# Kernel tuning notes

Hardware: AMD Instinct MI355X
Metric: run time of the kernel (lower is better)

## Reference

```python
import math
import jax, jax.numpy as jnp
import numpy as np

NUM_LAYERS = 2
D = 128
H = 8
CTX = 16
B, M, T = 4, 16, 256


def _lin(x, W, b):
    # torch nn.Linear: y = x @ W^T + b, W: [out, in]
    return jnp.einsum('...d,ed->...e', x, W) + b


def _ln(x, g, b, eps=1e-6):
    mu = jnp.mean(x, axis=-1, keepdims=True)
    v = jnp.mean((x - mu) ** 2, axis=-1, keepdims=True)
    return (x - mu) / jnp.sqrt(v + eps) * g + b


def _context_attention(x, L):
    # Faithful vectorization of the per-position python loop in ContextAttention.
    # Zero left-padding is NOT masked in the softmax (pad keys give score 0),
    # exactly as in the torch original.
    b, m, t, d = x.shape
    xp = jnp.pad(x, ((0, 0), (0, 0), (L - 1, 0), (0, 0)))  # [b,m,t+L-1,d]
    idx = jnp.arange(t)[:, None] + jnp.arange(L)[None, :]   # [t,L] window indices
    win = xp[:, :, idx, :]                                  # [b,m,t,L,d]
    scores = jnp.einsum('bmtd,bmtld->bmtl', x, win) / math.sqrt(d)
    w = jax.nn.softmax(scores, axis=-1)
    return jnp.einsum('bmtl,bmtld->bmtd', w, win)


def setup_inputs():
    key = jax.random.key(0)
    ks = jax.random.split(key, 8)
    L = NUM_LAYERS

    def w(k, shape):
        return jax.random.normal(k, shape, dtype=jnp.float32) * 0.02

    return {
        'x': jax.random.normal(ks[0], (B, M, T, D), dtype=jnp.float32),
        'Wq': w(ks[1], (L, D, D)), 'bq': jnp.zeros((L, D), jnp.float32),
        'Wk': w(ks[2], (L, D, D)), 'bk': jnp.zeros((L, D), jnp.float32),
        'Wv': w(ks[3], (L, D, D)), 'bv': jnp.zeros((L, D), jnp.float32),
        'Wo': w(ks[4], (L, D, D)), 'bo': jnp.zeros((L, D), jnp.float32),
        'W1': w(ks[5], (L, 4 * D, D)), 'b1': jnp.zeros((L, 4 * D), jnp.float32),
        'W2': w(ks[6], (L, D, 4 * D)), 'b2': jnp.zeros((L, D), jnp.float32),
        'ln1_g': jnp.ones((L, D), jnp.float32), 'ln1_b': jnp.zeros((L, D), jnp.float32),
        'ln2_g': jnp.ones((L, D), jnp.float32), 'ln2_b': jnp.zeros((L, D), jnp.float32),
        'lnf_g': jnp.ones((D,), jnp.float32), 'lnf_b': jnp.zeros((D,), jnp.float32),
        'context_len': CTX,
    }


def reference(x, Wq, bq, Wk, bk, Wv, bv, Wo, bo, W1, b1, W2, b2,
              ln1_g, ln1_b, ln2_g, ln2_b, lnf_g, lnf_b, context_len):
    b, m, t, d = x.shape
    dk = d // H

    def mha(xin, i):
        q = _lin(xin, Wq[i], bq[i])
        k = _lin(xin, Wk[i], bk[i])
        v = _lin(xin, Wv[i], bv[i])
        cq = _context_attention(q, context_len).reshape(b, m, t, H, dk)
        ck = _context_attention(k, context_len).reshape(b, m, t, H, dk)
        vr = v.reshape(b, m, t, H, dk)
        # full attention over time axis
        s = jnp.einsum('bmqhd,bmkhd->bmhqk', cq, ck) / math.sqrt(dk)
        xa = jnp.einsum('bmhqk,bmkhd->bmqhd', jax.nn.softmax(s, axis=-1), vr)
        # relational attention over the asset axis m
        s2 = jnp.einsum('bqthd,bkthd->bthqk', xa, xa) / math.sqrt(dk)
        xr = jnp.einsum('bthqk,bkthd->bthqd', jax.nn.softmax(s2, axis=-1), xa)
        # torch: permute((3,0,1,2,4)) -> [m,b,t,h,dk], then .view(b,m,t,d)
        xr = jnp.transpose(xr, (3, 0, 1, 2, 4)).reshape(b, m, t, d)
        return _lin(xr, Wo[i], bo[i])

    def ffn(xin, i):
        return _lin(jax.nn.relu(_lin(xin, W1[i], b1[i])), W2[i], b2[i])

    y = x
    for i in range(Wq.shape[0]):
        y = y + mha(_ln(y, ln1_g[i], ln1_b[i]), i)
        y = y + ffn(_ln(y, ln2_g[i], ln2_b[i]), i)
    return _ln(y, lnf_g, lnf_b)
```

## Files before the change

### kernel.cpp

```cpp
#include <hip/hip_runtime.h>
#include <cstddef>
#include <cstdint>

static constexpr int D_ = 128;
static constexpr int NROW = 16384;
static constexpr size_t S_ = (size_t)NROW * D_;

typedef __attribute__((ext_vector_type(8))) short bf16x8;
typedef __attribute__((ext_vector_type(4))) float f32x4;
typedef __attribute__((ext_vector_type(16))) float f32x16;
typedef __attribute__((ext_vector_type(8))) unsigned short ushortx8;
typedef __attribute__((ext_vector_type(4))) unsigned short ushortx4;

__device__ __forceinline__ unsigned short f2bf(float f) {
  unsigned int u = __float_as_uint(f);
  u += 0x7fff + ((u >> 16) & 1);
  return (unsigned short)(u >> 16);
}
__device__ __forceinline__ float bf2f(unsigned short h) {
  return __uint_as_float(((unsigned int)h) << 16);
}
__device__ __forceinline__ unsigned int cvt_pk_bf16(float lo, float hi) {
  unsigned int r;
  asm volatile("v_cvt_pk_bf16_f32 %0, %1, %2" : "=v"(r) : "v"(lo), "v"(hi));
  return r;
}
__device__ __forceinline__ float wsum64(float s) {
#pragma unroll
  for (int off = 32; off >= 1; off >>= 1) s += __shfl_xor(s, off);
  return s;
}

__global__ __launch_bounds__(256) void lnconv_kernel(
    const float* __restrict__ X, const float* __restrict__ g,
    const float* __restrict__ b, unsigned short* __restrict__ out) {
  int wid = threadIdx.x >> 6, lane = threadIdx.x & 63;
  int row = (blockIdx.x << 2) + wid;
  float2 xv = *(const float2*)(X + (size_t)row * D_ + lane * 2);
  float s = wsum64(xv.x + xv.y);
  float sq = wsum64(xv.x * xv.x + xv.y * xv.y);
  float mu = s * (1.0f / 128.0f);
  float var = sq * (1.0f / 128.0f) - mu * mu;
  float rstd = rsqrtf(var + 1e-6f);
  float2 gv = *(const float2*)(g + lane * 2);
  float2 bv = *(const float2*)(b + lane * 2);
  unsigned int lo = f2bf((xv.x - mu) * rstd * gv.x + bv.x);
  unsigned int hi = f2bf((xv.y - mu) * rstd * gv.y + bv.y);
  *(unsigned int*)(out + (size_t)row * D_ + lane * 2) = lo | (hi << 16);
}

__global__ __launch_bounds__(256) void wconv_kernel(
    const float* __restrict__ Wq, const float* __restrict__ Wk,
    const float* __restrict__ Wv, const float* __restrict__ Wo,
    const float* __restrict__ W1, const float* __restrict__ W2,
    unsigned short* __restrict__ out) {
  size_t i = ((size_t)blockIdx.x * 256 + threadIdx.x) * 8;
  int layer = i >= 196608;
  size_t o = i - (size_t)layer * 196608;
  const float* src; size_t off;
  if      (o < 16384)  { src = Wq + layer * 16384; off = o; }
  else if (o < 32768)  { src = Wk + layer * 16384; off = o - 16384; }
  else if (o < 49152)  { src = Wv + layer * 16384; off = o - 32768; }
  else if (o < 65536)  { src = Wo + layer * 16384; off = o - 49152; }
  else if (o < 131072) { src = W1 + layer * 65536; off = o - 65536; }
  else                 { src = W2 + layer * 65536; off = o - 131072; }
  ushortx8 r;
#pragma unroll
  for (int j = 0; j < 8; j++) r[j] = f2bf(src[off + j]);
  *(ushortx8*)(out + i) = r;
}

__global__ __launch_bounds__(256) void bconv_kernel(
    const float* __restrict__ bq, const float* __restrict__ bk,
    const float* __restrict__ bv, const float* __restrict__ bo,
    const float* __restrict__ b1, const float* __restrict__ b2,
    float* __restrict__ out) {
  int tid = threadIdx.x + blockIdx.x * 256;
  if (tid >= 2304) return;
  int layer = tid / 1152, o = tid % 1152;
  float v;
  if      (o < 128)  v = bq[layer * 128 + o];
  else if (o < 256)  v = bk[layer * 128 + o - 128];
  else if (o < 384)  v = bv[layer * 128 + o - 256];
  else if (o < 512)  v = bo[layer * 128 + o - 384];
  else if (o < 1024) v = b1[layer * 512 + o - 512];
  else               v = b2[layer * 128 + o - 1024];
  out[tid] = v;
}

template <int NT, int ROWW>
__global__ __launch_bounds__(512, 2) void gemm_kernel(
    const unsigned short* __restrict__ A, int lda,
    const unsigned short* __restrict__ W, int ldw,
    const float* __restrict__ bias,
    unsigned short* __restrict__ Cb, int K) {
  constexpr int COLW = 8 / ROWW;
  const int w = threadIdx.x >> 6;
  const int l = threadIdx.x & 63;
  const int rw = w / COLW, cw = w % COLW;
  const int r0 = blockIdx.x * (16 * ROWW) + rw * 16;
  const int c0 = cw * (NT * 16);
  const int lr = l & 15, lk = (l >> 4) * 8;
  f32x4 acc[NT] = {};
  const unsigned short* Ap = A + (size_t)(r0 + lr) * lda + lk;
  const unsigned short* Wp = W + (size_t)(c0 + lr) * ldw + lk;
  for (int kb = 0; kb < K; kb += 128) {
    bf16x8 aF[4];
    bf16x8 wF[4][NT];
#pragma unroll
    for (int kt = 0; kt < 4; ++kt) {
      int k0 = kb + kt * 32;
      aF[kt] = *(const bf16x8*)(Ap + k0);
#pragma unroll
      for (int n = 0; n < NT; ++n)
        wF[kt][n] = *(const bf16x8*)(Wp + (size_t)(n * 16) * ldw + k0);
    }
#pragma unroll
    for (int kt = 0; kt < 4; ++kt)
#pragma unroll
      for (int n = 0; n < NT; ++n)
        acc[n] = __builtin_amdgcn_mfma_f32_16x16x32_bf16(aF[kt], wF[kt][n], acc[n], 0, 0, 0);
  }
  const int rb = (l >> 4) * 4;
#pragma unroll
  for (int n = 0; n < NT; ++n) {
    int col = c0 + n * 16 + lr;
    float bval = bias[col];
    unsigned short* dst = Cb + (size_t)(col >> 7) * S_ + (col & 127);
#pragma unroll
    for (int j = 0; j < 4; ++j)
      dst[(size_t)(r0 + rb + j) * 128] = f2bf(acc[n][j] + bval);
  }
}

static constexpr int LDH = 136;
__global__ __launch_bounds__(512, 2) void ffn_kernel(
    const unsigned short* __restrict__ Abuf,
    const unsigned short* __restrict__ Wo_, const unsigned short* __restrict__ W1_,
    const unsigned short* __restrict__ W2_, const float* __restrict__ Bl,
    const float* __restrict__ rin,
    const float* __restrict__ ln2G, const float* __restrict__ ln2B,
    const float* __restrict__ lnxG, const float* __restrict__ lnxB,
    float* __restrict__ Yout, unsigned short* __restrict__ AbOut, int finalMode) {
  __shared__ unsigned short As[64][LDH];
  __shared__ unsigned short Hs[64][LDH];
  __shared__ unsigned short Mid[64][LDH];
  __shared__ float2 lnred[64][8];
  const int tid = threadIdx.x;
  const int w = tid >> 6, l = tid & 63;
  const int r0 = blockIdx.x * 64;
  const int lr = l & 15, lk = (l >> 4) * 8, rb = (l >> 4) * 4;
  const int col = w * 16 + lr;

  bf16x8 wof[4], w1f[4], w2f[4];
#pragma unroll
  for (int kt = 0; kt < 4; ++kt) {
    wof[kt] = *(const bf16x8*)(Wo_ + (size_t)col * 128 + kt * 32 + lk);
    w1f[kt] = *(const bf16x8*)(W1_ + (size_t)col * 128 + kt * 32 + lk);
    w2f[kt] = *(const bf16x8*)(W2_ + (size_t)col * 512 + kt * 32 + lk);
  }
#pragma unroll
  for (int itr = 0; itr < 2; ++itr) {
    int idx = itr * 512 + tid;
    int r = idx >> 4, c8 = (idx & 15) * 8;
    *(ushortx8*)&As[r][c8] = *(const ushortx8*)(Abuf + (size_t)(r0 + r) * 128 + c8);
  }
  __syncthreads();

  f32x4 acc1[4] = {};
#pragma unroll
  for (int kt = 0; kt < 4; ++kt)
#pragma unroll
    for (int m = 0; m < 4; ++m) {
      bf16x8 a = *(const bf16x8*)&As[m * 16 + lr][kt * 32 + lk];
      acc1[m] = __builtin_amdgcn_mfma_f32_16x16x32_bf16(a, wof[kt], acc1[m], 0, 0, 0);
    }
  float yreg[4][4];
  {
    float bval = Bl[384 + col];
#pragma unroll
    for (int m = 0; m < 4; ++m)
#pragma unroll
      for (int j = 0; j < 4; ++j)
        yreg[m][j] = acc1[m][j] + bval + rin[(size_t)(r0 + m * 16 + rb + j) * 128 + col];
  }
  {
    float s[4][4], sq[4][4];
#pragma unroll
    for (int m = 0; m < 4; ++m)
#pragma unroll
      for (int j = 0; j < 4; ++j) { s[m][j] = yreg[m][j]; sq[m][j] = yreg[m][j] * yreg[m][j]; }
#pragma unroll
    for (int off = 1; off < 16; off <<= 1)
#pragma unroll
      for (int m = 0; m < 4; ++m)
#pragma unroll
        for (int j = 0; j < 4; ++j) {
          s[m][j] += __shfl_xor(s[m][j], off);
          sq[m][j] += __shfl_xor(sq[m][j], off);
        }
    if (lr == 0)
#pragma unroll
      for (int m = 0; m < 4; ++m)
#pragma unroll
        for (int j = 0; j < 4; ++j)
          lnred[m * 16 + rb + j][w] = make_float2(s[m][j], sq[m][j]);
    __syncthreads();
    if (tid < 64) {
      float ts = 0.f, tq = 0.f;
#pragma unroll
      for (int k = 0; k < 8; ++k) { float2 p = lnred[tid][k]; ts += p.x; tq += p.y; }
      float mu = ts * (1.0f / 128.0f);
      float rstd = rsqrtf(tq * (1.0f / 128.0f) - mu * mu + 1e-6f);
      lnred[tid][0] = make_float2(mu, rstd);
    }
    __syncthreads();
    float g = ln2G[col], bb = ln2B[col];
#pragma unroll
    for (int m = 0; m < 4; ++m)
#pragma unroll
      for (int j = 0; j < 4; ++j) {
        float2 st = lnred[m * 16 + rb + j][0];
        Hs[m * 16 + rb + j][col] = f2bf((yreg[m][j] - st.x) * st.y * g + bb);
      }
  }
  __syncthreads();
  f32x4 acc2[4] = {};
#pragma unroll
  for (int c = 0; c < 4; ++c) {
    bf16x8 w1n[4], w2n[4];
    if (c < 3) {
#pragma unroll
      for (int kt = 0; kt < 4; ++kt) {
        w1n[kt] = *(const bf16x8*)(W1_ + (size_t)((c + 1) * 128 + col) * 128 + kt * 32 + lk);
        w2n[kt] = *(const bf16x8*)(W2_ + (size_t)col * 512 + (c + 1) * 128 + kt * 32 + lk);
      }
    }
    f32x4 accm[4] = {};
#pragma unroll
    for (int kt = 0; kt < 4; ++kt)
#pragma unroll
      for (int m = 0; m < 4; ++m) {
        bf16x8 a = *(const bf16x8*)&Hs[m * 16 + lr][kt * 32 + lk];
        accm[m] = __builtin_amdgcn_mfma_f32_16x16x32_bf16(a, w1f[kt], accm[m], 0, 0, 0);
      }
    float b1v = Bl[512 + c * 128 + col];
#pragma unroll
    for (int m = 0; m < 4; ++m)
#pragma unroll
      for (int j = 0; j < 4; ++j)
        Mid[m * 16 + rb + j][col] = f2bf(fmaxf(accm[m][j] + b1v, 0.f));
    __syncthreads();
#pragma unroll
    for (int kt = 0; kt < 4; ++kt)
#pragma unroll
      for (int m = 0; m < 4; ++m) {
        bf16x8 a = *(const bf16x8*)&Mid[m * 16 + lr][kt * 32 + lk];
        acc2[m] = __builtin_amdgcn_mfma_f32_16x16x32_bf16(a, w2f[kt], acc2[m], 0, 0, 0);
      }
    __syncthreads();
    if (c < 3) {
#pragma unroll
      for (int kt = 0; kt < 4; ++kt) { w1f[kt] = w1n[kt]; w2f[kt] = w2n[kt]; }
    }
  }
  float vfin[4][4];
  {
    float bval = Bl[1024 + col];
    float s[4][4], sq[4][4];
#pragma unroll
    for (int m = 0; m < 4; ++m)
#pragma unroll
      for (int j = 0; j < 4; ++j) {
        float v = acc2[m][j] + bval + yreg[m][j];
        vfin[m][j] = v;
        s[m][j] = v;
        sq[m][j] = v * v;
      }
#pragma unroll
    for (int off = 1; off < 16; off <<= 1)
#pragma unroll
      for (int m = 0; m < 4; ++m)
#pragma unroll
        for (int j = 0; j < 4; ++j) {
          s[m][j] += __shfl_xor(s[m][j], off);
          sq[m][j] += __shfl_xor(sq[m][j], off);
        }
    if (lr == 0)
#pragma unroll
      for (int m = 0; m < 4; ++m)
#pragma unroll
        for (int j = 0; j < 4; ++j)
          lnred[m * 16 + rb + j][w] = make_float2(s[m][j], sq[m][j]);
    __syncthreads();
    if (tid < 64) {
      float ts = 0.f, tq = 0.f;
#pragma unroll
      for (int k = 0; k < 8; ++k) { float2 p = lnred[tid][k]; ts += p.x; tq += p.y; }
      float mu = ts * (1.0f / 128.0f);
      float rstd = rsqrtf(tq * (1.0f / 128.0f) - mu * mu + 1e-6f);
      lnred[tid][0] = make_float2(mu, rstd);
    }
    __syncthreads();
    float g = lnxG[col], bb = lnxB[col];
#pragma unroll
    for (int m = 0; m < 4; ++m)
#pragma unroll
      for (int j = 0; j < 4; ++j) {
        int row = r0 + m * 16 + rb + j;
        float2 st = lnred[m * 16 + rb + j][0];
        float t = (vfin[m][j] - st.x) * st.y * g + bb;
        if (finalMode == 0) {
          Yout[(size_t)row * 128 + col] = vfin[m][j];
          AbOut[(size_t)row * 128 + col] = f2bf(t);
        } else {
          Yout[(size_t)row * 128 + col] = t;
        }
      }
  }
}

static constexpr int CTXLD = 130;
__global__ __launch_bounds__(128) void ctx_kernel(
    const unsigned short* __restrict__ qin, const unsigned short* __restrict__ kin,
    unsigned short* __restrict__ cqo, unsigned short* __restrict__ cko) {
  __shared__ float xs[79 * CTXLD];
  const unsigned short* src = blockIdx.y ? kin : qin;
  unsigned short* dst = blockIdx.y ? cko : cqo;
  const size_t rbase = (size_t)blockIdx.x * 256;
  const int t0 = blockIdx.z * 64;
  const int tid = threadIdx.x;
#pragma unroll
  for (int it = 0; it < 10; ++it) {
    int idx = it * 128 + tid;
    int i = idx >> 4, c8 = (idx & 15) * 8;
    if (i < 79) {
      int rg = t0 - 15 + i;
      float f[8];
      if (rg >= 0) {
        ushortx8 wv = *(const ushortx8*)(src + (rbase + rg) * 128 + c8);
#pragma unroll
        for (int j = 0; j < 8; ++j) f[j] = bf2f(wv[j]);
      } else {
#pragma unroll
        for (int j = 0; j < 8; ++j) f[j] = 0.f;
      }
#pragma unroll
      for (int j = 0; j < 8; j += 2)
        *(float2*)&xs[i * CTXLD + c8 + j] = make_float2(f[j], f[j + 1]);
    }
  }
  __syncthreads();
  const int ql = tid >> 1, h = tid & 1;
  const int cb = h * 64;
  float ow[64];
#pragma unroll
  for (int c = 0; c < 64; c += 2) {
    float2 w = *(const float2*)&xs[(ql + 15) * CTXLD + cb + c];
    ow[c] = w.x; ow[c + 1] = w.y;
  }
  float p[16];
#pragma unroll
  for (int l = 0; l < 16; ++l) {
    const float* row = &xs[(ql + l) * CTXLD + cb];
    float d = 0.f;
#pragma unroll
    for (int c = 0; c < 64; c += 2) {
      float2 w = *(const float2*)(row + c);
      d = fmaf(ow[c], w.x, d);
      d = fmaf(ow[c + 1], w.y, d);
    }
    p[l] = d;
  }
  float den = 0.f;
#pragma unroll
  for (int l = 0; l < 16; ++l) {
    float sc = p[l] + __shfl_xor(p[l], 1);
    p[l] = __expf(sc * 0.08838834764831845f);
    den += p[l];
  }
  float o[64];
#pragma unroll
  for (int c = 0; c < 64; ++c) o[c] = 0.f;
#pragma unroll
  for (int l = 0; l < 16; ++l) {
    float pl = p[l];
    const float* row = &xs[(ql + l) * CTXLD + cb];
#pragma unroll
    for (int c = 0; c < 64; c += 2) {
      float2 w = *(const float2*)(row + c);
      o[c] = fmaf(pl, w.x, o[c]);
      o[c + 1] = fmaf(pl, w.y, o[c + 1]);
    }
  }
  float inv = 1.0f / den;
  unsigned short* op = dst + (rbase + t0 + ql) * 128 + cb;
#pragma unroll
  for (int c8 = 0; c8 < 8; ++c8) {
    ushortx8 r;
#pragma unroll
    for (int j = 0; j < 8; ++j) r[j] = f2bf(o[c8 * 8 + j] * inv);
    *(ushortx8*)(op + c8 * 8) = r;
  }
}

static constexpr int PW = 272;
__global__ __launch_bounds__(256) void attn1_kernel(
    const unsigned short* __restrict__ cq, const unsigned short* __restrict__ ck,
    unsigned short* __restrict__ v) {
  __shared__ unsigned short vt[16][PW];
  __shared__ unsigned short ps[4][32][PW];
  __shared__ float rsum[4][32];
  const int bm = blockIdx.x >> 3, h = blockIdx.x & 7;
  const size_t rbase = (size_t)bm * 256;
  const int cbase = h * 16;
  const int tid = threadIdx.x;
  {
    ushortx8 v0 = *(const ushortx8*)(v + (rbase + tid) * 128 + cbase);
    ushortx8 v1 = *(const ushortx8*)(v + (rbase + tid) * 128 + cbase + 8);
#pragma unroll
    for (int d = 0; d < 8; ++d) { vt[d][tid] = v0[d]; vt[8 + d][tid] = v1[d]; }
  }
  __syncthreads();
  const int wid = tid >> 6, lane = tid & 63;
  const int l31 = lane & 31, l15 = lane & 15;
  const int hi5 = lane >> 5, hi4 = lane >> 4;
#pragma unroll
  for (int qt = 0; qt < 2; ++qt) {
    const int q0 = (wid * 2 + qt) * 32;
    bf16x8 bq = *(const bf16x8*)(cq + (rbase + q0 + l31) * 128 + cbase + hi5 * 8);
    float lsum = 0.f;
#pragma unroll
    for (int kt = 0; kt < 8; ++kt) {
      bf16x8 ak = *(const bf16x8*)(ck + (rbase + kt * 32 + l31) * 128 + cbase + hi5 * 8);
      f32x16 z = {};
      f32x16 s = __builtin_amdgcn_mfma_f32_32x32x16_bf16(ak, bq, z, 0, 0, 0);
      float p[16];
#pragma unroll
      for (int r = 0; r < 16; ++r) { p[r] = __expf(s[r] * 0.25f); lsum += p[r]; }
#pragma unroll
      for (int r = 0; r < 16; r += 2) {
        unsigned int pk = cvt_pk_bf16(p[r], p[r + 1]);
        int key = kt * 32 + (r & 3) + 8 * (r >> 2) + 4 * hi5;
        *(unsigned int*)&ps[wid][l31][key] = pk;
      }
    }
    lsum += __shfl_xor(lsum, 32);
    if (lane < 32) rsum[wid][lane] = 1.0f / lsum;
#pragma unroll
    for (int m = 0; m < 2; ++m) {
      f32x4 o = {};
#pragma unroll
      for (int k2 = 0; k2 < 8; ++k2) {
        bf16x8 pa = *(const bf16x8*)&ps[wid][m * 16 + l15][k2 * 32 + hi4 * 8];
        bf16x8 vb = *(const bf16x8*)&vt[l15][k2 * 32 + hi4 * 8];
        o = __builtin_amdgcn_mfma_f32_16x16x32_bf16(pa, vb, o, 0, 0, 0);
      }
      unsigned short* dst = v + (rbase + q0 + m * 16 + hi4 * 4) * 128 + cbase + l15;
#pragma unroll
      for (int j = 0; j < 4; ++j) {
        float inv = rsum[wid][m * 16 + hi4 * 4 + j];
        dst[(size_t)j * 128] = f2bf(o[j] * inv);
      }
    }
  }
}

__global__ __launch_bounds__(128) void attn2_kernel(
    const unsigned short* __restrict__ xa, unsigned short* __restrict__ xr) {
  __shared__ float xas[16][128];
  int b = blockIdx.x >> 8, t = blockIdx.x & 255;
  int tid = threadIdx.x;
#pragma unroll
  for (int jj = 0; jj < 2; ++jj) {
    int idx = tid + (jj << 7);
    int r = idx >> 4, c8 = (idx & 15) * 8;
    ushortx8 vv = *(const ushortx8*)(xa + ((size_t)((b * 16 + r) * 256 + t)) * 128 + c8);
#pragma unroll
    for (int j = 0; j < 8; ++j) xas[r][c8 + j] = bf2f(vv[j]);
  }
  __syncthreads();
  int h = tid >> 4, q = tid & 15;
  float xq[16];
#pragma unroll
  for (int d = 0; d < 16; d++) xq[d] = xas[q][h * 16 + d];
  float sc[16];
  float mx = -1e30f;
#pragma unroll
  for (int k = 0; k < 16; k++) {
    float s = 0.f;
#pragma unroll
    for (int d = 0; d < 16; d++) s += xq[d] * xas[k][h * 16 + d];
    s *= 0.25f;
    sc[k] = s;
    mx = fmaxf(mx, s);
  }
  float den = 0.f;
#pragma unroll
  for (int k = 0; k < 16; k++) { sc[k] = __expf(sc[k] - mx); den += sc[k]; }
  float inv = 1.0f / den;
  float out[16] = {};
#pragma unroll
  for (int k = 0; k < 16; k++) {
    float w = sc[k];
#pragma unroll
    for (int d = 0; d < 16; d++) out[d] += w * xas[k][h * 16 + d];
  }
  int g = q * 4 + b;
  unsigned short* dstp = xr + ((size_t)(g * 256 + t)) * 128 + h * 16;
  ushortx8 r0;
#pragma unroll
  for (int j = 0; j < 8; ++j) r0[j] = f2bf(out[j] * inv);
  *(ushortx8*)dstp = r0;
#pragma unroll
  for (int j = 0; j < 8; ++j) r0[j] = f2bf(out[8 + j] * inv);
  *(ushortx8*)(dstp + 8) = r0;
}

extern "C" void kernel_launch(void* const* d_in, const int* in_sizes, int n_in,
                              void* d_out, int out_size, void* d_ws, size_t ws_size,
                              hipStream_t stream) {
  const float* x    = (const float*)d_in[0];
  const float* Wq   = (const float*)d_in[1];
  const float* bq   = (const float*)d_in[2];
  const float* Wk   = (const float*)d_in[3];
  const float* bk   = (const float*)d_in[4];
  const float* Wv   = (const float*)d_in[5];
  const float* bv   = (const float*)d_in[6];
  const float* Wo   = (const float*)d_in[7];
  const float* bo   = (const float*)d_in[8];
  const float* W1   = (const float*)d_in[9];
  const float* b1   = (const float*)d_in[10];
  const float* W2   = (const float*)d_in[11];
  const float* b2   = (const float*)d_in[12];
  const float* ln1g = (const float*)d_in[13];
  const float* ln1b = (const float*)d_in[14];
  const float* ln2g = (const float*)d_in[15];
  const float* ln2b = (const float*)d_in[16];
  const float* lnfg = (const float*)d_in[17];
  const float* lnfb = (const float*)d_in[18];

  char* base = (char*)d_ws;
  unsigned short* CQb = (unsigned short*)base;
  unsigned short* CKb = (unsigned short*)(base + (4u  << 20));
  unsigned short* Qb  = (unsigned short*)(base + (8u  << 20));
  unsigned short* Kb  = (unsigned short*)(base + (12u << 20));
  unsigned short* Vb  = (unsigned short*)(base + (16u << 20));
  unsigned short* Ab  = (unsigned short*)(base + (20u << 20));
  unsigned short* Wb  = (unsigned short*)(base + (24u << 20));
  float*          Bs  = (float*)(base + (24u << 20) + 786432);
  float*          Y   = (float*)d_out;

  wconv_kernel<<<192, 256, 0, stream>>>(Wq, Wk, Wv, Wo, W1, W2, Wb);
  bconv_kernel<<<9, 256, 0, stream>>>(bq, bk, bv, bo, b1, b2, Bs);
  lnconv_kernel<<<4096, 256, 0, stream>>>(x, ln1g, ln1b, Ab);

  for (int i = 0; i < 2; ++i) {
    const float* rin = i ? Y : x;
    const unsigned short* Wl = Wb + (size_t)i * 196608;
    const float* Bl = Bs + i * 1152;
    gemm_kernel<6, 2><<<512, 512, 0, stream>>>(Ab, 128, Wl, 128, Bl, Qb, 128);
    ctx_kernel<<<dim3(64, 2, 4), 128, 0, stream>>>(Qb, Kb, CQb, CKb);
    attn1_kernel<<<512, 256, 0, stream>>>(CQb, CKb, Vb);
    attn2_kernel<<<1024, 128, 0, stream>>>(Vb, Ab);
    if (i == 0) {
      ffn_kernel<<<256, 512, 0, stream>>>(Ab, Wl + 49152, Wl + 65536, Wl + 131072, Bl,
          rin, ln2g, ln2b, ln1g + 128, ln1b + 128, Y, Ab, 0);
    } else {
      ffn_kernel<<<256, 512, 0, stream>>>(Ab, Wl + 49152, Wl + 65536, Wl + 131072, Bl,
          rin, ln2g + 128, ln2b + 128, lnfg, lnfb, Y, nullptr, 1);
    }
  }
}
```

Baseline: 187.7 us.

## Merge prep kernels, split ctx work finer, and shrink QKV GEMM tiles

Folds the weight, bias and LayerNorm conversion kernels into one prep kernel launch, which removes two launches. The context-attention kernel now covers 32 timesteps per block instead of 64 and uses four threads per query instead of two, with padded shared-memory rows to avoid bank conflicts, so twice as many blocks run with fewer registers each. The QKV GEMM switches to a smaller tile configuration with twice the grid size to raise occupancy. The cost is more redundant halo loads in the context kernel, an extra shuffle reduction, and less reuse per GEMM tile.

```diff
diff --git a/kernel.cpp b/kernel.cpp
--- a/kernel.cpp
+++ b/kernel.cpp
@@ -10,7 +10,6 @@
 typedef __attribute__((ext_vector_type(4))) float f32x4;
 typedef __attribute__((ext_vector_type(16))) float f32x16;
 typedef __attribute__((ext_vector_type(8))) unsigned short ushortx8;
-typedef __attribute__((ext_vector_type(4))) unsigned short ushortx4;
 
 __device__ __forceinline__ unsigned short f2bf(float f) {
   unsigned int u = __float_as_uint(f);
@@ -31,61 +30,60 @@
   return s;
 }
 
-__global__ __launch_bounds__(256) void lnconv_kernel(
-    const float* __restrict__ X, const float* __restrict__ g,
-    const float* __restrict__ b, unsigned short* __restrict__ out) {
-  int wid = threadIdx.x >> 6, lane = threadIdx.x & 63;
-  int row = (blockIdx.x << 2) + wid;
-  float2 xv = *(const float2*)(X + (size_t)row * D_ + lane * 2);
-  float s = wsum64(xv.x + xv.y);
-  float sq = wsum64(xv.x * xv.x + xv.y * xv.y);
-  float mu = s * (1.0f / 128.0f);
-  float var = sq * (1.0f / 128.0f) - mu * mu;
-  float rstd = rsqrtf(var + 1e-6f);
-  float2 gv = *(const float2*)(g + lane * 2);
-  float2 bv = *(const float2*)(b + lane * 2);
-  unsigned int lo = f2bf((xv.x - mu) * rstd * gv.x + bv.x);
-  unsigned int hi = f2bf((xv.y - mu) * rstd * gv.y + bv.y);
-  *(unsigned int*)(out + (size_t)row * D_ + lane * 2) = lo | (hi << 16);
-}
-
-__global__ __launch_bounds__(256) void wconv_kernel(
+__global__ __launch_bounds__(256) void prep_kernel(
+    const float* __restrict__ X,
     const float* __restrict__ Wq, const float* __restrict__ Wk,
     const float* __restrict__ Wv, const float* __restrict__ Wo,
     const float* __restrict__ W1, const float* __restrict__ W2,
-    unsigned short* __restrict__ out) {
-  size_t i = ((size_t)blockIdx.x * 256 + threadIdx.x) * 8;
-  int layer = i >= 196608;
-  size_t o = i - (size_t)layer * 196608;
-  const float* src; size_t off;
-  if      (o < 16384)  { src = Wq + layer * 16384; off = o; }
-  else if (o < 32768)  { src = Wk + layer * 16384; off = o - 16384; }
-  else if (o < 49152)  { src = Wv + layer * 16384; off = o - 32768; }
-  else if (o < 65536)  { src = Wo + layer * 16384; off = o - 49152; }
-  else if (o < 131072) { src = W1 + layer * 65536; off = o - 65536; }
-  else                 { src = W2 + layer * 65536; off = o - 131072; }
-  ushortx8 r;
-#pragma unroll
-  for (int j = 0; j < 8; j++) r[j] = f2bf(src[off + j]);
-  *(ushortx8*)(out + i) = r;
-}
-
-__global__ __launch_bounds__(256) void bconv_kernel(
     const float* __restrict__ bq, const float* __restrict__ bk,
     const float* __restrict__ bv, const float* __restrict__ bo,
     const float* __restrict__ b1, const float* __restrict__ b2,
-    float* __restrict__ out) {
-  int tid = threadIdx.x + blockIdx.x * 256;
-  if (tid >= 2304) return;
-  int layer = tid / 1152, o = tid % 1152;
-  float v;
-  if      (o < 128)  v = bq[layer * 128 + o];
-  else if (o < 256)  v = bk[layer * 128 + o - 128];
-  else if (o < 384)  v = bv[layer * 128 + o - 256];
-  else if (o < 512)  v = bo[layer * 128 + o - 384];
-  else if (o < 1024) v = b1[layer * 512 + o - 512];
-  else               v = b2[layer * 128 + o - 1024];
-  out[tid] = v;
+    const float* __restrict__ g, const float* __restrict__ b,
+    unsigned short* __restrict__ Wb, float* __restrict__ Bs,
+    unsigned short* __restrict__ Ab) {
+  int bx = blockIdx.x;
+  if (bx < 192) {
+    size_t i = ((size_t)bx * 256 + threadIdx.x) * 8;
+    int layer = i >= 196608;
+    size_t o = i - (size_t)layer * 196608;
+    const float* src; size_t off;
+    if      (o < 16384)  { src = Wq + layer * 16384; off = o; }
+    else if (o < 32768)  { src = Wk + layer * 16384; off = o - 16384; }
+    else if (o < 49152)  { src = Wv + layer * 16384; off = o - 32768; }
+    else if (o < 65536)  { src = Wo + layer * 16384; off = o - 49152; }
+    else if (o < 131072) { src = W1 + layer * 65536; off = o - 65536; }
+    else                 { src = W2 + layer * 65536; off = o - 131072; }
+    ushortx8 r;
+#pragma unroll
+    for (int j = 0; j < 8; j++) r[j] = f2bf(src[off + j]);
+    *(ushortx8*)(Wb + i) = r;
+  } else if (bx < 201) {
+    int tid = (bx - 192) * 256 + threadIdx.x;
+    if (tid >= 2304) return;
+    int layer = tid / 1152, o = tid % 1152;
+    float v;
+    if      (o < 128)  v = bq[layer * 128 + o];
+    else if (o < 256)  v = bk[layer * 128 + o - 128];
+    else if (o < 384)  v = bv[layer * 128 + o - 256];
+    else if (o < 512)  v = bo[layer * 128 + o - 384];
+    else if (o < 1024) v = b1[layer * 512 + o - 512];
+    else               v = b2[layer * 128 + o - 1024];
+    Bs[tid] = v;
+  } else {
+    int wid = threadIdx.x >> 6, lane = threadIdx.x & 63;
+    int row = ((bx - 201) << 2) + wid;
+    float2 xv = *(const float2*)(X + (size_t)row * D_ + lane * 2);
+    float s = wsum64(xv.x + xv.y);
+    float sq = wsum64(xv.x * xv.x + xv.y * xv.y);
+    float mu = s * (1.0f / 128.0f);
+    float var = sq * (1.0f / 128.0f) - mu * mu;
+    float rstd = rsqrtf(var + 1e-6f);
+    float2 gv = *(const float2*)(g + lane * 2);
+    float2 bv2 = *(const float2*)(b + lane * 2);
+    unsigned int lo = f2bf((xv.x - mu) * rstd * gv.x + bv2.x);
+    unsigned int hi = f2bf((xv.y - mu) * rstd * gv.y + bv2.y);
+    *(unsigned int*)(Ab + (size_t)row * D_ + lane * 2) = lo | (hi << 16);
+  }
 }
 
 template <int NT, int ROWW>
@@ -320,21 +318,21 @@
   }
 }
 
-static constexpr int CTXLD = 130;
+static constexpr int CTXLD = 134;
 __global__ __launch_bounds__(128) void ctx_kernel(
     const unsigned short* __restrict__ qin, const unsigned short* __restrict__ kin,
     unsigned short* __restrict__ cqo, unsigned short* __restrict__ cko) {
-  __shared__ float xs[79 * CTXLD];
+  __shared__ float xs[47 * CTXLD];
   const unsigned short* src = blockIdx.y ? kin : qin;
   unsigned short* dst = blockIdx.y ? cko : cqo;
   const size_t rbase = (size_t)blockIdx.x * 256;
-  const int t0 = blockIdx.z * 64;
+  const int t0 = blockIdx.z * 32;
   const int tid = threadIdx.x;
 #pragma unroll
-  for (int it = 0; it < 10; ++it) {
+  for (int it = 0; it < 6; ++it) {
     int idx = it * 128 + tid;
     int i = idx >> 4, c8 = (idx & 15) * 8;
-    if (i < 79) {
+    if (i < 47) {
       int rg = t0 - 15 + i;
       float f[8];
       if (rg >= 0) {
@@ -345,17 +343,19 @@
 #pragma unroll
         for (int j = 0; j < 8; ++j) f[j] = 0.f;
       }
+      int base = i * CTXLD + c8 + (c8 >> 5) * 2;
 #pragma unroll
       for (int j = 0; j < 8; j += 2)
-        *(float2*)&xs[i * CTXLD + c8 + j] = make_float2(f[j], f[j + 1]);
+        *(float2*)&xs[base + j] = make_float2(f[j], f[j + 1]);
     }
   }
   __syncthreads();
-  const int ql = tid >> 1, h = tid & 1;
-  const int cb = h * 64;
-  float ow[64];
-#pragma unroll
-  for (int c = 0; c < 64; c += 2) {
+  const int ql = tid >> 2, qu = tid & 3;
+  const int cb = qu * 34;
+  const int cg = qu * 32;
+  float ow[32];
+#pragma unroll
+  for (int c = 0; c < 32; c += 2) {
     float2 w = *(const float2*)&xs[(ql + 15) * CTXLD + cb + c];
     ow[c] = w.x; ow[c + 1] = w.y;
   }
@@ -365,7 +365,7 @@
     const float* row = &xs[(ql + l) * CTXLD + cb];
     float d = 0.f;
 #pragma unroll
-    for (int c = 0; c < 64; c += 2) {
+    for (int c = 0; c < 32; c += 2) {
       float2 w = *(const float2*)(row + c);
       d = fmaf(ow[c], w.x, d);
       d = fmaf(ow[c + 1], w.y, d);
@@ -376,27 +376,28 @@
 #pragma unroll
   for (int l = 0; l < 16; ++l) {
     float sc = p[l] + __shfl_xor(p[l], 1);
+    sc += __shfl_xor(sc, 2);
     p[l] = __expf(sc * 0.08838834764831845f);
     den += p[l];
   }
-  float o[64];
-#pragma unroll
-  for (int c = 0; c < 64; ++c) o[c] = 0.f;
+  float o[32];
+#pragma unroll
+  for (int c = 0; c < 32; ++c) o[c] = 0.f;
 #pragma unroll
   for (int l = 0; l < 16; ++l) {
     float pl = p[l];
     const float* row = &xs[(ql + l) * CTXLD + cb];
 #pragma unroll
-    for (int c = 0; c < 64; c += 2) {
+    for (int c = 0; c < 32; c += 2) {
       float2 w = *(const float2*)(row + c);
       o[c] = fmaf(pl, w.x, o[c]);
       o[c + 1] = fmaf(pl, w.y, o[c + 1]);
     }
   }
   float inv = 1.0f / den;
-  unsigned short* op = dst + (rbase + t0 + ql) * 128 + cb;
-#pragma unroll
-  for (int c8 = 0; c8 < 8; ++c8) {
+  unsigned short* op = dst + (rbase + t0 + ql) * 128 + cg;
+#pragma unroll
+  for (int c8 = 0; c8 < 4; ++c8) {
     ushortx8 r;
 #pragma unroll
     for (int j = 0; j < 8; ++j) r[j] = f2bf(o[c8 * 8 + j] * inv);
@@ -551,16 +552,16 @@
   float*          Bs  = (float*)(base + (24u << 20) + 786432);
   float*          Y   = (float*)d_out;
 
-  wconv_kernel<<<192, 256, 0, stream>>>(Wq, Wk, Wv, Wo, W1, W2, Wb);
-  bconv_kernel<<<9, 256, 0, stream>>>(bq, bk, bv, bo, b1, b2, Bs);
-  lnconv_kernel<<<4096, 256, 0, stream>>>(x, ln1g, ln1b, Ab);
+  prep_kernel<<<4297, 256, 0, stream>>>(x, Wq, Wk, Wv, Wo, W1, W2,
+                                        bq, bk, bv, bo, b1, b2,
+                                        ln1g, ln1b, Wb, Bs, Ab);
 
   for (int i = 0; i < 2; ++i) {
     const float* rin = i ? Y : x;
     const unsigned short* Wl = Wb + (size_t)i * 196608;
     const float* Bl = Bs + i * 1152;
-    gemm_kernel<6, 2><<<512, 512, 0, stream>>>(Ab, 128, Wl, 128, Bl, Qb, 128);
-    ctx_kernel<<<dim3(64, 2, 4), 128, 0, stream>>>(Qb, Kb, CQb, CKb);
+    gemm_kernel<3, 1><<<1024, 512, 0, stream>>>(Ab, 128, Wl, 128, Bl, Qb, 128);
+    ctx_kernel<<<dim3(64, 2, 8), 128, 0, stream>>>(Qb, Kb, CQb, CKb);
     attn1_kernel<<<512, 256, 0, stream>>>(CQb, CKb, Vb);
     attn2_kernel<<<1024, 128, 0, stream>>>(Vb, Ab);
     if (i == 0) {
```

New measurement: 186.9 us. About the same (-0.4%).
